# Kernel optimization log

Measured on AMD Instinct MI355X. Metric: run time of the kernel, lower is better.

The kernel has to match this reference:

```python
import jax, jax.numpy as jnp
import numpy as np

B, T, C, H = 2, 2048, 1024, 16
HD = C // H  # head dim = 64


def setup_inputs() -> dict:
    key = jax.random.key(0)
    ks = jax.random.split(key, 5)
    s = 0.02
    return {
        "x": jax.random.normal(ks[0], (B, T, C), dtype=jnp.float32),
        "w_attn": jax.random.normal(ks[1], (C, 3 * C), dtype=jnp.float32) * s,
        "b_attn": jnp.zeros((3 * C,), dtype=jnp.float32),
        "w_proj": jax.random.normal(ks[2], (C, C), dtype=jnp.float32) * s,
        "b_proj": jnp.zeros((C,), dtype=jnp.float32),
    }


def reference(x, w_attn, b_attn, w_proj, b_proj):
    Bc, Tc, Cc = x.shape
    qkv = x @ w_attn + b_attn                      # [B,T,3C]
    q, k, v = jnp.split(qkv, 3, axis=2)            # each [B,T,C]
    # [B,T,C] -> [B,H,T,HD]
    def heads(t):
        return t.reshape(Bc, Tc, H, HD).transpose(0, 2, 1, 3)
    q, k, v = heads(q), heads(k), heads(v)
    scale = 1.0 / jnp.sqrt(jnp.asarray(HD, dtype=x.dtype))
    att = jnp.einsum("bhqd,bhkd->bhqk", q, k) * scale   # [B,H,T,T]
    causal = jnp.tril(jnp.ones((Tc, Tc), dtype=bool))
    att = jnp.where(causal, att, jnp.asarray(-jnp.inf, dtype=att.dtype))
    att = jax.nn.softmax(att, axis=-1)
    y = jnp.einsum("bhqk,bhkd->bhqd", att, v)            # [B,H,T,HD]
    y = y.transpose(0, 2, 1, 3).reshape(Bc, Tc, Cc)      # [B,T,C]
    return y @ w_proj + b_proj
```

## Files before the change

kernel.cpp:

```cpp
#include <hip/hip_runtime.h>
#include <stdint.h>


typedef short bf16x8 __attribute__((ext_vector_type(8)));
typedef float f32x4 __attribute__((ext_vector_type(4)));

__device__ inline unsigned short f2bf(float f) {
  union { float f; uint32_t u; } v; v.f = f;
  uint32_t u = v.u;
  u += 0x7FFFu + ((u >> 16) & 1u);
  return (unsigned short)(u >> 16);
}

__device__ inline void load_lds16(const unsigned short* g, unsigned short* l) {
  __builtin_amdgcn_global_load_lds(
      (const __attribute__((address_space(1))) unsigned int*)(const void*)g,
      (__attribute__((address_space(3))) unsigned int*)(void*)l, 16, 0, 0);
}

__global__ __launch_bounds__(256) void cast_bf16_kernel(
    const float* __restrict__ in, unsigned short* __restrict__ out, int n4) {
  int i = blockIdx.x * 256 + threadIdx.x;
  if (i >= n4) return;
  float4 f = reinterpret_cast<const float4*>(in)[i];
  ushort4 o;
  o.x = f2bf(f.x); o.y = f2bf(f.y); o.z = f2bf(f.z); o.w = f2bf(f.w);
  reinterpret_cast<ushort4*>(out)[i] = o;
}

__global__ void transpose_cast_kernel(
    const float* __restrict__ in, unsigned short* __restrict__ out, int R, int Cn) {
  __shared__ float tile[32][33];
  int bx = blockIdx.x * 32, by = blockIdx.y * 32;
  int tx = threadIdx.x, ty = threadIdx.y;
  #pragma unroll
  for (int i = 0; i < 32; i += 8)
    tile[ty + i][tx] = in[(size_t)(by + ty + i) * Cn + bx + tx];
  __syncthreads();
  #pragma unroll
  for (int i = 0; i < 32; i += 8)
    out[(size_t)(bx + ty + i) * R + by + tx] = f2bf(tile[tx][ty + i]);
}

__global__ __launch_bounds__(256) void vtrans_kernel(
    const unsigned short* __restrict__ qkv, unsigned short* __restrict__ vt) {
  __shared__ unsigned short Ts[64][72];
  const int bh = blockIdx.y, kt = blockIdx.x;
  const unsigned short* vb = qkv + ((size_t)(64 + bh) * 2048) * 64;
  const int t = threadIdx.x;
  const int key = t >> 2, c0 = (t & 3) * 2;
  #pragma unroll
  for (int j = 0; j < 2; ++j) {
    uint4 u = *reinterpret_cast<const uint4*>(vb + (size_t)(kt * 64 + key) * 64 + (c0 + j) * 8);
    *reinterpret_cast<uint4*>(&Ts[key][(c0 + j) * 8]) = u;
  }
  __syncthreads();
  const int d = t >> 2;
  #pragma unroll
  for (int j = 0; j < 2; ++j) {
    int kc = c0 + j;
    ushort4 a, b;
    unsigned short* pa = reinterpret_cast<unsigned short*>(&a);
    unsigned short* pb = reinterpret_cast<unsigned short*>(&b);
    #pragma unroll
    for (int kk = 0; kk < 4; ++kk) pa[kk] = Ts[kc * 8 + kk][d];
    #pragma unroll
    for (int kk = 0; kk < 4; ++kk) pb[kk] = Ts[kc * 8 + 4 + kk][d];
    unsigned short* dst = vt + ((size_t)bh * 64 + d) * 2048 + kt * 64 + kc * 8;
    *reinterpret_cast<ushort4*>(dst) = a;
    *reinterpret_cast<ushort4*>(dst + 4) = b;
  }
}

__global__ __launch_bounds__(256) void gemm_bt_kernel(
    const unsigned short* __restrict__ A,
    const unsigned short* __restrict__ Bt,
    const float* __restrict__ bias,
    void* __restrict__ outp,
    int M, int N, int K, int mode) {
  __shared__ unsigned short As[128 * 32];
  __shared__ unsigned short Bs[128 * 32];
  const int t = threadIdx.x;
  const int wave = t >> 6, lane = t & 63;
  const int L = lane & 15, quad = lane >> 4;
  const int wm = (wave >> 1) * 64, wn = (wave & 1) * 64;
  const int m0 = blockIdx.y * 128, n0 = blockIdx.x * 128;

  const int drow = lane >> 2;
  const int dch  = (lane & 3) ^ (drow & 3);
  const int foff = ((quad ^ (L & 3)) * 8);

  f32x4 acc[4][4] = {};

  for (int k0 = 0; k0 < K; k0 += 32) {
    __syncthreads();
    #pragma unroll
    for (int j = 0; j < 2; ++j) {
      int r0 = wave * 32 + j * 16;
      load_lds16(A  + (size_t)(m0 + r0 + drow) * K + k0 + dch * 8, &As[r0 * 32]);
      load_lds16(Bt + (size_t)(n0 + r0 + drow) * K + k0 + dch * 8, &Bs[r0 * 32]);
    }
    __syncthreads();
    bf16x8 af[4], bf[4];
    #pragma unroll
    for (int mt = 0; mt < 4; ++mt)
      af[mt] = *reinterpret_cast<const bf16x8*>(&As[(wm + mt * 16 + L) * 32 + foff]);
    #pragma unroll
    for (int nt = 0; nt < 4; ++nt)
      bf[nt] = *reinterpret_cast<const bf16x8*>(&Bs[(wn + nt * 16 + L) * 32 + foff]);
    #pragma unroll
    for (int mt = 0; mt < 4; ++mt)
      #pragma unroll
      for (int nt = 0; nt < 4; ++nt)
        acc[mt][nt] = __builtin_amdgcn_mfma_f32_16x16x32_bf16(af[mt], bf[nt], acc[mt][nt], 0, 0, 0);
  }

  if (mode == 0) {
    float* out = (float*)outp;
    #pragma unroll
    for (int mt = 0; mt < 4; ++mt)
      #pragma unroll
      for (int nt = 0; nt < 4; ++nt) {
        int col = n0 + wn + nt * 16 + L;
        float b = bias[col];
        #pragma unroll
        for (int r = 0; r < 4; ++r) {
          int row = m0 + wm + mt * 16 + quad * 4 + r;
          out[(size_t)row * N + col] = acc[mt][nt][r] + b;
        }
      }
  } else {
    unsigned short* qkv = (unsigned short*)outp;
    #pragma unroll
    for (int mt = 0; mt < 4; ++mt)
      #pragma unroll
      for (int nt = 0; nt < 4; ++nt) {
        int col = n0 + wn + nt * 16 + L;
        int sel = col >> 10, cc = col & 1023;
        int h = cc >> 6, d = cc & 63;
        float b = bias[col];
        float sc = (sel == 0) ? 0.18033688011112042f : 1.0f;
        #pragma unroll
        for (int r = 0; r < 4; ++r) {
          int row = m0 + wm + mt * 16 + quad * 4 + r;
          int bb = row >> 11, tt = row & 2047;
          float val = (acc[mt][nt][r] + b) * sc;
          qkv[(((size_t)sel * 32 + (size_t)(bb * 16 + h)) * 2048 + tt) * 64 + d] = f2bf(val);
        }
      }
  }
}

__global__ __launch_bounds__(256) void attn_kernel(
    const unsigned short* __restrict__ qkv,
    const unsigned short* __restrict__ vt,
    unsigned short* __restrict__ y) {
  __shared__ unsigned short Ks[64 * 64];
  __shared__ unsigned short Vs[64 * 64];
  __shared__ unsigned short Ps[4][32][68];

  const int t = threadIdx.x;
  const int wave = t >> 6, lane = t & 63;
  const int L = lane & 15, quad = lane >> 4;
  const int bh = blockIdx.y;
  const int i  = blockIdx.x;
  const int tA = i, tB = 31 - i;
  const int rowA0 = tA * 64 + wave * 16;
  const int rowB0 = tB * 64 + wave * 16;
  const int ntiles = tB + 1;

  const unsigned short* qb  = qkv + ((size_t)bh * 2048) * 64;
  const unsigned short* kb  = qkv + ((size_t)(32 + bh) * 2048) * 64;
  const unsigned short* vtb = vt + (size_t)bh * 64 * 2048;

  const int drow = lane >> 3;
  const int dch  = (lane & 7) ^ drow;
  const int fo[2] = { ((quad ^ (L & 7)) * 8), (((quad + 4) ^ (L & 7)) * 8) };

  bf16x8 qfA[2], qfB[2];
  #pragma unroll
  for (int h = 0; h < 2; ++h) {
    qfA[h] = *reinterpret_cast<const bf16x8*>(qb + (size_t)(rowA0 + L) * 64 + h * 32 + quad * 8);
    qfB[h] = *reinterpret_cast<const bf16x8*>(qb + (size_t)(rowB0 + L) * 64 + h * 32 + quad * 8);
  }

  f32x4 oA[4] = {}, oB[4] = {};
  float rsA[4] = {}, rsB[4] = {};

  for (int kt = 0; kt < ntiles; ++kt) {
    __syncthreads();
    {
      const int kg = kt * 64;
      #pragma unroll
      for (int j = 0; j < 2; ++j) {
        int r0 = wave * 16 + j * 8;
        load_lds16(kb  + (size_t)(kg + r0 + drow) * 64 + dch * 8, &Ks[r0 * 64]);
        load_lds16(vtb + (size_t)(r0 + drow) * 2048 + kg + dch * 8, &Vs[r0 * 64]);
      }
    }
    __syncthreads();

    const bool actA = (kt <= tA);

    bf16x8 kf[4][2];
    #pragma unroll
    for (int nt = 0; nt < 4; ++nt)
      #pragma unroll
      for (int h = 0; h < 2; ++h)
        kf[nt][h] = *reinterpret_cast<const bf16x8*>(&Ks[(nt * 16 + L) * 64 + fo[h]]);

    f32x4 sB[4] = {};
    #pragma unroll
    for (int nt = 0; nt < 4; ++nt)
      #pragma unroll
      for (int h = 0; h < 2; ++h)
        sB[nt] = __builtin_amdgcn_mfma_f32_16x16x32_bf16(qfB[h], kf[nt][h], sB[nt], 0, 0, 0);

    if (kt == tB) {
      #pragma unroll
      for (int nt = 0; nt < 4; ++nt) {
        int key = kt * 64 + nt * 16 + L;
        #pragma unroll
        for (int r = 0; r < 4; ++r)
          if (key > rowB0 + quad * 4 + r) sB[nt][r] = -3.0e38f;
      }
    }
    #pragma unroll
    for (int nt = 0; nt < 4; ++nt)
      #pragma unroll
      for (int r = 0; r < 4; ++r) {
        float p = exp2f(sB[nt][r]);
        rsB[r] += p;
        Ps[wave][16 + quad * 4 + r][nt * 16 + L] = f2bf(p);
      }

    if (actA) {
      f32x4 sA[4] = {};
      #pragma unroll
      for (int nt = 0; nt < 4; ++nt)
        #pragma unroll
        for (int h = 0; h < 2; ++h)
          sA[nt] = __builtin_amdgcn_mfma_f32_16x16x32_bf16(qfA[h], kf[nt][h], sA[nt], 0, 0, 0);
      if (kt == tA) {
        #pragma unroll
        for (int nt = 0; nt < 4; ++nt) {
          int key = kt * 64 + nt * 16 + L;
          #pragma unroll
          for (int r = 0; r < 4; ++r)
            if (key > rowA0 + quad * 4 + r) sA[nt][r] = -3.0e38f;
        }
      }
      #pragma unroll
      for (int nt = 0; nt < 4; ++nt)
        #pragma unroll
        for (int r = 0; r < 4; ++r) {
          float p = exp2f(sA[nt][r]);
          rsA[r] += p;
          Ps[wave][quad * 4 + r][nt * 16 + L] = f2bf(p);
        }
    }

    bf16x8 vf[4][2];
    #pragma unroll
    for (int nt = 0; nt < 4; ++nt)
      #pragma unroll
      for (int h = 0; h < 2; ++h)
        vf[nt][h] = *reinterpret_cast<const bf16x8*>(&Vs[(nt * 16 + L) * 64 + fo[h]]);

    bf16x8 pb0 = *reinterpret_cast<const bf16x8*>(&Ps[wave][16 + L][quad * 8]);
    bf16x8 pb1 = *reinterpret_cast<const bf16x8*>(&Ps[wave][16 + L][32 + quad * 8]);
    #pragma unroll
    for (int nt = 0; nt < 4; ++nt) {
      oB[nt] = __builtin_amdgcn_mfma_f32_16x16x32_bf16(pb0, vf[nt][0], oB[nt], 0, 0, 0);
      oB[nt] = __builtin_amdgcn_mfma_f32_16x16x32_bf16(pb1, vf[nt][1], oB[nt], 0, 0, 0);
    }
    if (actA) {
      bf16x8 pa0 = *reinterpret_cast<const bf16x8*>(&Ps[wave][L][quad * 8]);
      bf16x8 pa1 = *reinterpret_cast<const bf16x8*>(&Ps[wave][L][32 + quad * 8]);
      #pragma unroll
      for (int nt = 0; nt < 4; ++nt) {
        oA[nt] = __builtin_amdgcn_mfma_f32_16x16x32_bf16(pa0, vf[nt][0], oA[nt], 0, 0, 0);
        oA[nt] = __builtin_amdgcn_mfma_f32_16x16x32_bf16(pa1, vf[nt][1], oA[nt], 0, 0, 0);
      }
    }
  }

  float invA[4], invB[4];
  #pragma unroll
  for (int r = 0; r < 4; ++r) {
    float a = rsA[r], b = rsB[r];
    #pragma unroll
    for (int off = 1; off < 16; off <<= 1) {
      a += __shfl_xor(a, off, 64);
      b += __shfl_xor(b, off, 64);
    }
    invA[r] = 1.0f / a;
    invB[r] = 1.0f / b;
  }
  const int bb = bh >> 4, hh = bh & 15;
  #pragma unroll
  for (int nt = 0; nt < 4; ++nt)
    #pragma unroll
    for (int r = 0; r < 4; ++r) {
      int rA = rowA0 + quad * 4 + r;
      int rB = rowB0 + quad * 4 + r;
      int col = hh * 64 + nt * 16 + L;
      y[((size_t)bb * 2048 + rA) * 1024 + col] = f2bf(oA[nt][r] * invA[r]);
      y[((size_t)bb * 2048 + rB) * 1024 + col] = f2bf(oB[nt][r] * invB[r]);
    }
}

extern "C" void kernel_launch(void* const* d_in, const int* in_sizes, int n_in,
                              void* d_out, int out_size, void* d_ws, size_t ws_size,
                              hipStream_t stream) {
  const float* x      = (const float*)d_in[0];
  const float* w_attn = (const float*)d_in[1];
  const float* b_attn = (const float*)d_in[2];
  const float* w_proj = (const float*)d_in[3];
  const float* b_proj = (const float*)d_in[4];
  float* out = (float*)d_out;

  unsigned short* ws = (unsigned short*)d_ws;
  unsigned short* xb     = ws;
  unsigned short* wattnT = xb + 4194304;
  unsigned short* wprojT = wattnT + 3145728;
  unsigned short* qkv    = wprojT + 1048576;
  unsigned short* yb     = qkv + 12582912;
  unsigned short* vt     = yb + 4194304;

  cast_bf16_kernel<<<4096, 256, 0, stream>>>(x, xb, 1048576);
  transpose_cast_kernel<<<dim3(96, 32), dim3(32, 8), 0, stream>>>(w_attn, wattnT, 1024, 3072);
  transpose_cast_kernel<<<dim3(32, 32), dim3(32, 8), 0, stream>>>(w_proj, wprojT, 1024, 1024);

  gemm_bt_kernel<<<dim3(24, 32), 256, 0, stream>>>(xb, wattnT, b_attn, qkv, 4096, 3072, 1024, 1);
  vtrans_kernel<<<dim3(32, 32), 256, 0, stream>>>(qkv, vt);
  attn_kernel<<<dim3(16, 32), 256, 0, stream>>>(qkv, vt, yb);
  gemm_bt_kernel<<<dim3(8, 32), 256, 0, stream>>>(yb, wprojT, b_proj, out, 4096, 1024, 1024, 0);
}
```

Baseline: 219.2 us.

## Triple-buffer attention K/V loads, fuse V transpose into QKV GEMM epilogue

The attention kernel now prefetches the next K/V tile into a three-slot LDS ring, using a waitcnt plus barrier instead of two full syncthreads per tile. QK^T is computed transposed so each lane holds four consecutive keys, which allows packed bf16 conversion, vector stores of P and a simpler row-sum reduction. The separate V-transpose kernel is removed: the QKV GEMM epilogue writes V directly in transposed layout, though those stores are strided. The GEMM LDS swizzle is also changed. This removes one launch and one pass over V, and hides load latency in attention at the cost of more LDS.

```diff
diff --git a/kernel.cpp b/kernel.cpp
--- a/kernel.cpp
+++ b/kernel.cpp
@@ -10,6 +10,16 @@
   uint32_t u = v.u;
   u += 0x7FFFu + ((u >> 16) & 1u);
   return (unsigned short)(u >> 16);
+}
+
+__device__ inline unsigned pkbf(float a, float b) {
+#if __has_builtin(__builtin_amdgcn_cvt_pk_bf16_f32)
+  typedef __bf16 v2bf __attribute__((ext_vector_type(2)));
+  v2bf v = __builtin_amdgcn_cvt_pk_bf16_f32(a, b);
+  unsigned u; __builtin_memcpy(&u, &v, 4); return u;
+#else
+  return (unsigned)f2bf(a) | ((unsigned)f2bf(b) << 16);
+#endif
 }
 
 __device__ inline void load_lds16(const unsigned short* g, unsigned short* l) {
@@ -42,41 +52,12 @@
     out[(size_t)(bx + ty + i) * R + by + tx] = f2bf(tile[tx][ty + i]);
 }
 
-__global__ __launch_bounds__(256) void vtrans_kernel(
-    const unsigned short* __restrict__ qkv, unsigned short* __restrict__ vt) {
-  __shared__ unsigned short Ts[64][72];
-  const int bh = blockIdx.y, kt = blockIdx.x;
-  const unsigned short* vb = qkv + ((size_t)(64 + bh) * 2048) * 64;
-  const int t = threadIdx.x;
-  const int key = t >> 2, c0 = (t & 3) * 2;
-  #pragma unroll
-  for (int j = 0; j < 2; ++j) {
-    uint4 u = *reinterpret_cast<const uint4*>(vb + (size_t)(kt * 64 + key) * 64 + (c0 + j) * 8);
-    *reinterpret_cast<uint4*>(&Ts[key][(c0 + j) * 8]) = u;
-  }
-  __syncthreads();
-  const int d = t >> 2;
-  #pragma unroll
-  for (int j = 0; j < 2; ++j) {
-    int kc = c0 + j;
-    ushort4 a, b;
-    unsigned short* pa = reinterpret_cast<unsigned short*>(&a);
-    unsigned short* pb = reinterpret_cast<unsigned short*>(&b);
-    #pragma unroll
-    for (int kk = 0; kk < 4; ++kk) pa[kk] = Ts[kc * 8 + kk][d];
-    #pragma unroll
-    for (int kk = 0; kk < 4; ++kk) pb[kk] = Ts[kc * 8 + 4 + kk][d];
-    unsigned short* dst = vt + ((size_t)bh * 64 + d) * 2048 + kt * 64 + kc * 8;
-    *reinterpret_cast<ushort4*>(dst) = a;
-    *reinterpret_cast<ushort4*>(dst + 4) = b;
-  }
-}
-
 __global__ __launch_bounds__(256) void gemm_bt_kernel(
     const unsigned short* __restrict__ A,
     const unsigned short* __restrict__ Bt,
     const float* __restrict__ bias,
     void* __restrict__ outp,
+    unsigned short* __restrict__ vtp,
     int M, int N, int K, int mode) {
   __shared__ unsigned short As[128 * 32];
   __shared__ unsigned short Bs[128 * 32];
@@ -87,8 +68,8 @@
   const int m0 = blockIdx.y * 128, n0 = blockIdx.x * 128;
 
   const int drow = lane >> 2;
-  const int dch  = (lane & 3) ^ (drow & 3);
-  const int foff = ((quad ^ (L & 3)) * 8);
+  const int dch  = (lane & 3) ^ ((drow >> 1) & 3);
+  const int foff = ((quad ^ ((L >> 1) & 3)) * 8);
 
   f32x4 acc[4][4] = {};
 
@@ -145,7 +126,11 @@
           int row = m0 + wm + mt * 16 + quad * 4 + r;
           int bb = row >> 11, tt = row & 2047;
           float val = (acc[mt][nt][r] + b) * sc;
-          qkv[(((size_t)sel * 32 + (size_t)(bb * 16 + h)) * 2048 + tt) * 64 + d] = f2bf(val);
+          if (sel == 2) {
+            vtp[((size_t)(bb * 16 + h) * 64 + d) * 2048 + tt] = f2bf(val);
+          } else {
+            qkv[(((size_t)sel * 32 + (size_t)(bb * 16 + h)) * 2048 + tt) * 64 + d] = f2bf(val);
+          }
         }
       }
   }
@@ -155,16 +140,16 @@
     const unsigned short* __restrict__ qkv,
     const unsigned short* __restrict__ vt,
     unsigned short* __restrict__ y) {
-  __shared__ unsigned short Ks[64 * 64];
-  __shared__ unsigned short Vs[64 * 64];
-  __shared__ unsigned short Ps[4][32][68];
+  __shared__ unsigned short Ks[3][64 * 64];
+  __shared__ unsigned short Vs[3][64 * 64];
+  __shared__ unsigned short Ps[4][32][72];
 
   const int t = threadIdx.x;
   const int wave = t >> 6, lane = t & 63;
   const int L = lane & 15, quad = lane >> 4;
   const int bh = blockIdx.y;
-  const int i  = blockIdx.x;
-  const int tA = i, tB = 31 - i;
+  const int pi = blockIdx.x;
+  const int tA = pi, tB = 31 - pi;
   const int rowA0 = tA * 64 + wave * 16;
   const int rowB0 = tB * 64 + wave * 16;
   const int ntiles = tB + 1;
@@ -175,7 +160,8 @@
 
   const int drow = lane >> 3;
   const int dch  = (lane & 7) ^ drow;
-  const int fo[2] = { ((quad ^ (L & 7)) * 8), (((quad + 4) ^ (L & 7)) * 8) };
+  const int fo0 = ((quad ^ (L & 7)) * 8);
+  const int fo1 = (((quad + 4) ^ (L & 7)) * 8);
 
   bf16x8 qfA[2], qfB[2];
   #pragma unroll
@@ -185,88 +171,106 @@
   }
 
   f32x4 oA[4] = {}, oB[4] = {};
-  float rsA[4] = {}, rsB[4] = {};
-
+  float rsA = 0.f, rsB = 0.f;
+
+  {
+    #pragma unroll
+    for (int j = 0; j < 2; ++j) {
+      int r0 = wave * 16 + j * 8;
+      load_lds16(kb  + (size_t)(0 + r0 + drow) * 64 + dch * 8, &Ks[0][r0 * 64]);
+      load_lds16(vtb + (size_t)(r0 + drow) * 2048 + 0 + dch * 8, &Vs[0][r0 * 64]);
+    }
+  }
+
+  int buf = 0;
   for (int kt = 0; kt < ntiles; ++kt) {
-    __syncthreads();
+    const int nkt = (kt + 1 < ntiles) ? kt + 1 : ntiles - 1;
+    const int nbuf = (buf == 2) ? 0 : buf + 1;
     {
-      const int kg = kt * 64;
+      const int kg = nkt * 64;
       #pragma unroll
       for (int j = 0; j < 2; ++j) {
         int r0 = wave * 16 + j * 8;
-        load_lds16(kb  + (size_t)(kg + r0 + drow) * 64 + dch * 8, &Ks[r0 * 64]);
-        load_lds16(vtb + (size_t)(r0 + drow) * 2048 + kg + dch * 8, &Vs[r0 * 64]);
-      }
-    }
-    __syncthreads();
+        load_lds16(kb  + (size_t)(kg + r0 + drow) * 64 + dch * 8, &Ks[nbuf][r0 * 64]);
+        load_lds16(vtb + (size_t)(r0 + drow) * 2048 + kg + dch * 8, &Vs[nbuf][r0 * 64]);
+      }
+    }
+    asm volatile("" ::: "memory");
+    __builtin_amdgcn_s_waitcnt(0x0F74);
+    __builtin_amdgcn_s_barrier();
+    asm volatile("" ::: "memory");
 
     const bool actA = (kt <= tA);
 
     bf16x8 kf[4][2];
     #pragma unroll
-    for (int nt = 0; nt < 4; ++nt)
-      #pragma unroll
-      for (int h = 0; h < 2; ++h)
-        kf[nt][h] = *reinterpret_cast<const bf16x8*>(&Ks[(nt * 16 + L) * 64 + fo[h]]);
+    for (int nt = 0; nt < 4; ++nt) {
+      kf[nt][0] = *reinterpret_cast<const bf16x8*>(&Ks[buf][(nt * 16 + L) * 64 + fo0]);
+      kf[nt][1] = *reinterpret_cast<const bf16x8*>(&Ks[buf][(nt * 16 + L) * 64 + fo1]);
+    }
 
     f32x4 sB[4] = {};
     #pragma unroll
-    for (int nt = 0; nt < 4; ++nt)
-      #pragma unroll
-      for (int h = 0; h < 2; ++h)
-        sB[nt] = __builtin_amdgcn_mfma_f32_16x16x32_bf16(qfB[h], kf[nt][h], sB[nt], 0, 0, 0);
-
+    for (int nt = 0; nt < 4; ++nt) {
+      sB[nt] = __builtin_amdgcn_mfma_f32_16x16x32_bf16(kf[nt][0], qfB[0], sB[nt], 0, 0, 0);
+      sB[nt] = __builtin_amdgcn_mfma_f32_16x16x32_bf16(kf[nt][1], qfB[1], sB[nt], 0, 0, 0);
+    }
     if (kt == tB) {
       #pragma unroll
       for (int nt = 0; nt < 4; ++nt) {
-        int key = kt * 64 + nt * 16 + L;
+        int key0 = kt * 64 + nt * 16 + quad * 4;
+        int qr = rowB0 + L;
         #pragma unroll
         for (int r = 0; r < 4; ++r)
-          if (key > rowB0 + quad * 4 + r) sB[nt][r] = -3.0e38f;
-      }
-    }
-    #pragma unroll
-    for (int nt = 0; nt < 4; ++nt)
-      #pragma unroll
-      for (int r = 0; r < 4; ++r) {
-        float p = exp2f(sB[nt][r]);
-        rsB[r] += p;
-        Ps[wave][16 + quad * 4 + r][nt * 16 + L] = f2bf(p);
-      }
+          if (key0 + r > qr) sB[nt][r] = -3.0e38f;
+      }
+    }
+    #pragma unroll
+    for (int nt = 0; nt < 4; ++nt) {
+      float p0 = exp2f(sB[nt][0]), p1 = exp2f(sB[nt][1]);
+      float p2 = exp2f(sB[nt][2]), p3 = exp2f(sB[nt][3]);
+      rsB += (p0 + p1) + (p2 + p3);
+      uint2 pk;
+      pk.x = pkbf(p0, p1);
+      pk.y = pkbf(p2, p3);
+      *reinterpret_cast<uint2*>(&Ps[wave][16 + L][nt * 16 + quad * 4]) = pk;
+    }
 
     if (actA) {
       f32x4 sA[4] = {};
       #pragma unroll
-      for (int nt = 0; nt < 4; ++nt)
-        #pragma unroll
-        for (int h = 0; h < 2; ++h)
-          sA[nt] = __builtin_amdgcn_mfma_f32_16x16x32_bf16(qfA[h], kf[nt][h], sA[nt], 0, 0, 0);
+      for (int nt = 0; nt < 4; ++nt) {
+        sA[nt] = __builtin_amdgcn_mfma_f32_16x16x32_bf16(kf[nt][0], qfA[0], sA[nt], 0, 0, 0);
+        sA[nt] = __builtin_amdgcn_mfma_f32_16x16x32_bf16(kf[nt][1], qfA[1], sA[nt], 0, 0, 0);
+      }
       if (kt == tA) {
         #pragma unroll
         for (int nt = 0; nt < 4; ++nt) {
-          int key = kt * 64 + nt * 16 + L;
+          int key0 = kt * 64 + nt * 16 + quad * 4;
+          int qr = rowA0 + L;
           #pragma unroll
           for (int r = 0; r < 4; ++r)
-            if (key > rowA0 + quad * 4 + r) sA[nt][r] = -3.0e38f;
+            if (key0 + r > qr) sA[nt][r] = -3.0e38f;
         }
       }
       #pragma unroll
-      for (int nt = 0; nt < 4; ++nt)
-        #pragma unroll
-        for (int r = 0; r < 4; ++r) {
-          float p = exp2f(sA[nt][r]);
-          rsA[r] += p;
-          Ps[wave][quad * 4 + r][nt * 16 + L] = f2bf(p);
-        }
+      for (int nt = 0; nt < 4; ++nt) {
+        float p0 = exp2f(sA[nt][0]), p1 = exp2f(sA[nt][1]);
+        float p2 = exp2f(sA[nt][2]), p3 = exp2f(sA[nt][3]);
+        rsA += (p0 + p1) + (p2 + p3);
+        uint2 pk;
+        pk.x = pkbf(p0, p1);
+        pk.y = pkbf(p2, p3);
+        *reinterpret_cast<uint2*>(&Ps[wave][L][nt * 16 + quad * 4]) = pk;
+      }
     }
 
     bf16x8 vf[4][2];
     #pragma unroll
-    for (int nt = 0; nt < 4; ++nt)
-      #pragma unroll
-      for (int h = 0; h < 2; ++h)
-        vf[nt][h] = *reinterpret_cast<const bf16x8*>(&Vs[(nt * 16 + L) * 64 + fo[h]]);
-
+    for (int nt = 0; nt < 4; ++nt) {
+      vf[nt][0] = *reinterpret_cast<const bf16x8*>(&Vs[buf][(nt * 16 + L) * 64 + fo0]);
+      vf[nt][1] = *reinterpret_cast<const bf16x8*>(&Vs[buf][(nt * 16 + L) * 64 + fo1]);
+    }
     bf16x8 pb0 = *reinterpret_cast<const bf16x8*>(&Ps[wave][16 + L][quad * 8]);
     bf16x8 pb1 = *reinterpret_cast<const bf16x8*>(&Ps[wave][16 + L][32 + quad * 8]);
     #pragma unroll
@@ -283,19 +287,16 @@
         oA[nt] = __builtin_amdgcn_mfma_f32_16x16x32_bf16(pa1, vf[nt][1], oA[nt], 0, 0, 0);
       }
     }
-  }
-
+    buf = nbuf;
+  }
+
+  float a = rsA; a += __shfl_xor(a, 16, 64); a += __shfl_xor(a, 32, 64);
+  float b2 = rsB; b2 += __shfl_xor(b2, 16, 64); b2 += __shfl_xor(b2, 32, 64);
   float invA[4], invB[4];
   #pragma unroll
   for (int r = 0; r < 4; ++r) {
-    float a = rsA[r], b = rsB[r];
-    #pragma unroll
-    for (int off = 1; off < 16; off <<= 1) {
-      a += __shfl_xor(a, off, 64);
-      b += __shfl_xor(b, off, 64);
-    }
-    invA[r] = 1.0f / a;
-    invB[r] = 1.0f / b;
+    invA[r] = 1.0f / __shfl(a, quad * 4 + r, 64);
+    invB[r] = 1.0f / __shfl(b2, quad * 4 + r, 64);
   }
   const int bb = bh >> 4, hh = bh & 15;
   #pragma unroll
@@ -308,6 +309,7 @@
       y[((size_t)bb * 2048 + rA) * 1024 + col] = f2bf(oA[nt][r] * invA[r]);
       y[((size_t)bb * 2048 + rB) * 1024 + col] = f2bf(oB[nt][r] * invB[r]);
     }
+  __builtin_amdgcn_s_waitcnt(0);
 }
 
 extern "C" void kernel_launch(void* const* d_in, const int* in_sizes, int n_in,
@@ -332,8 +334,7 @@
   transpose_cast_kernel<<<dim3(96, 32), dim3(32, 8), 0, stream>>>(w_attn, wattnT, 1024, 3072);
   transpose_cast_kernel<<<dim3(32, 32), dim3(32, 8), 0, stream>>>(w_proj, wprojT, 1024, 1024);
 
-  gemm_bt_kernel<<<dim3(24, 32), 256, 0, stream>>>(xb, wattnT, b_attn, qkv, 4096, 3072, 1024, 1);
-  vtrans_kernel<<<dim3(32, 32), 256, 0, stream>>>(qkv, vt);
+  gemm_bt_kernel<<<dim3(24, 32), 256, 0, stream>>>(xb, wattnT, b_attn, qkv, vt, 4096, 3072, 1024, 1);
   attn_kernel<<<dim3(16, 32), 256, 0, stream>>>(qkv, vt, yb);
-  gemm_bt_kernel<<<dim3(8, 32), 256, 0, stream>>>(yb, wprojT, b_proj, out, 4096, 1024, 1024, 0);
-}
+  gemm_bt_kernel<<<dim3(8, 32), 256, 0, stream>>>(yb, wprojT, b_proj, out, nullptr, 4096, 1024, 1024, 0);
+}
```

Measured after the change: 205.9 us. 1.06x faster.
